# Performance work log

Hardware: AMD Instinct MI355X
Metric: run time of the kernel (lower is better)

The kernel has to match this reference:

```python
import jax, jax.numpy as jnp
import numpy as np

SIG_LEVEL = 2
UNIT = 128
SEQ = 64
BATCH = 256
SIG_DIM = UNIT + UNIT ** 2  # truncated signature dim for level 2
LN_EPS = 1e-5


def _signature(path, level):
    """Truncated path signature up to `level` via Chen's relation.
    path: (B, T, d) -> (B, d + d^2 + ... + d^level).
    Each segment contributes exp(dx): level-m term dx^{outer m}/m!.
    """
    B, T, d = path.shape
    dx = path[:, 1:] - path[:, :-1]  # (B, T-1, d)
    init = [jnp.zeros((B, d ** k), dtype=path.dtype) for k in range(1, level + 1)]

    def step(S, dxt):  # S: list of (B, d^k); dxt: (B, d)
        # P[m] = dxt^{outer m} / m!, flattened (B, d^m)
        P = [jnp.ones((B, 1), dtype=dxt.dtype), dxt]
        for m in range(2, level + 1):
            P.append((P[-1][:, :, None] * dxt[:, None, :]).reshape(B, d ** m) / m)
        newS = []
        for k in range(1, level + 1):
            s = P[k]  # j = 0 term (S_0 = 1)
            for j in range(1, k + 1):
                s = s + (S[j - 1][:, :, None] * P[k - j][:, None, :]).reshape(B, d ** k)
            newS.append(s)
        return newS, None

    S, _ = jax.lax.scan(step, init, jnp.swapaxes(dx, 0, 1))
    return jnp.concatenate(S, axis=-1)


def _grn_softmax(sig, W2, b2, W1, b1, Wg, bg, Wv, bv, Ws, bs, gamma, beta):
    # TFT-style gated residual network with softmax output activation.
    h = jax.nn.elu(sig @ W2 + b2)          # (B, unit)
    h = h @ W1 + b1                        # (B, unit)
    glu = jax.nn.sigmoid(h @ Wg + bg) * (h @ Wv + bv)
    skip = sig @ Ws + bs                   # residual projection sig_dim -> unit
    y = skip + glu
    mu = jnp.mean(y, axis=-1, keepdims=True)
    var = jnp.var(y, axis=-1, keepdims=True)
    y = (y - mu) * jax.lax.rsqrt(var + LN_EPS) * gamma + beta
    return jax.nn.softmax(y, axis=-1)


def setup_inputs() -> dict:
    key = jax.random.key(0)
    ks = jax.random.split(key, 16)
    s = 0.02
    return {
        "inputs": jax.random.normal(ks[0], (BATCH, SEQ, UNIT), dtype=jnp.float32),
        "time_kernel": jnp.ones((SEQ, 1), dtype=jnp.float32),
        "Wd": jax.random.normal(ks[1], (UNIT, UNIT), dtype=jnp.float32) * s,
        "bd": jnp.zeros((UNIT,), dtype=jnp.float32),
        "W2": jax.random.normal(ks[2], (SIG_DIM, UNIT), dtype=jnp.float32) * s,
        "b2": jnp.zeros((UNIT,), dtype=jnp.float32),
        "W1": jax.random.normal(ks[3], (UNIT, UNIT), dtype=jnp.float32) * s,
        "b1": jnp.zeros((UNIT,), dtype=jnp.float32),
        "Wg": jax.random.normal(ks[4], (UNIT, UNIT), dtype=jnp.float32) * s,
        "bg": jnp.zeros((UNIT,), dtype=jnp.float32),
        "Wv": jax.random.normal(ks[5], (UNIT, UNIT), dtype=jnp.float32) * s,
        "bv": jnp.zeros((UNIT,), dtype=jnp.float32),
        "Ws": jax.random.normal(ks[6], (SIG_DIM, UNIT), dtype=jnp.float32) * s,
        "bs": jnp.zeros((UNIT,), dtype=jnp.float32),
        "gamma": jnp.ones((UNIT,), dtype=jnp.float32),
        "beta": jnp.zeros((UNIT,), dtype=jnp.float32),
    }


def reference(inputs, time_kernel, Wd, bd, W2, b2, W1, b1, Wg, bg, Wv, bv, Ws, bs, gamma, beta):
    x = time_kernel * inputs                         # (B, T, d) time weighting
    sig = _signature(x, SIG_LEVEL)                   # (B, sig_dim)
    weights = _grn_softmax(sig, W2, b2, W1, b1, Wg, bg, Wv, bv, Ws, bs, gamma, beta)  # (B, d)
    dense_out = x @ Wd + bd                          # (B, T, d); dropout is identity at eval
    return dense_out * weights[:, None, :]
```

## Files before the change

kernel.cpp:

```cpp
#include <hip/hip_runtime.h>
#include <math.h>

#define SD 16512
#define NCH 129
#define CHUNKP 32768
#define LN_EPS 1e-5f

typedef __attribute__((ext_vector_type(4))) float f32x4;
typedef __attribute__((ext_vector_type(8))) short bf16x8;

__device__ __forceinline__ unsigned bfpack(float lo, float hi) {
    unsigned a = __builtin_bit_cast(unsigned, lo);
    unsigned b = __builtin_bit_cast(unsigned, hi);
    a = (a + 0x7FFFu + ((a >> 16) & 1u)) >> 16;
    b = (b + 0x7FFFu + ((b >> 16) & 1u)) >> 16;
    return a | (b << 16);
}
__device__ __forceinline__ unsigned short bf1(float x) {
    unsigned a = __builtin_bit_cast(unsigned, x);
    return (unsigned short)((a + 0x7FFFu + ((a >> 16) & 1u)) >> 16);
}

__global__ __launch_bounds__(512) void k_sig(const float* __restrict__ x,
                                             const float* __restrict__ tk,
                                             const float* __restrict__ Wd,
                                             unsigned short* __restrict__ sig,
                                             unsigned short* __restrict__ xbf,
                                             unsigned short* __restrict__ WdTg) {
    __shared__ unsigned short Ut[128][72];
    __shared__ unsigned short DXt[128][72];
    __shared__ float tks[64];
    int tid = threadIdx.x;
    int b = blockIdx.x;

    if (b == 256) {
        int d = tid & 127, kh = tid >> 7;
        unsigned* dst = (unsigned*)WdTg;
        for (int kk = 0; kk < 32; kk += 2) {
            int k = kh * 32 + kk;
            float v0 = Wd[(size_t)k * 128 + d];
            float v1 = Wd[(size_t)(k + 1) * 128 + d];
            dst[d * 64 + (k >> 1)] = bfpack(v0, v1);
        }
        return;
    }

    if (tid < 64) tks[tid] = tk[tid];
    __syncthreads();

    const float* xb = x + (size_t)b * 8192;
    unsigned short* xbb = xbf + (size_t)b * 8192;
    int i = tid & 127, th = tid >> 7;

    float x0 = tks[0] * xb[i];
    float xa = tks[th * 16] * xb[(size_t)(th * 16) * 128 + i];
    #pragma unroll
    for (int tp = 0; tp < 8; ++tp) {
        int p = th * 8 + tp;
        int t0 = 2 * p;
        float xv = tks[t0 + 1] * xb[(size_t)(t0 + 1) * 128 + i];
        float dx0 = xv - xa, u0 = 0.5f * (xa + xv) - x0;
        float dx1, u1, xc;
        if (p == 31) { dx1 = 0.f; u1 = 0.f; xc = 0.f; }
        else {
            xc = tks[t0 + 2] * xb[(size_t)(t0 + 2) * 128 + i];
            dx1 = xc - xv; u1 = 0.5f * (xv + xc) - x0;
        }
        *(unsigned*)&Ut[i][t0]  = bfpack(u0, u1);
        *(unsigned*)&DXt[i][t0] = bfpack(dx0, dx1);
        xbb[(size_t)t0 * 128 + i]       = bf1(xa);
        xbb[(size_t)(t0 + 1) * 128 + i] = bf1(xv);
        if (p == 31) sig[(size_t)b * SD + i] = bf1(xv - x0);
        xa = xc;
    }
    __syncthreads();

    int w = tid >> 6, lane = tid & 63;
    int wm = w >> 2, wn = w & 3;
    int l15 = lane & 15, lg = lane >> 4;
    f32x4 acc[4][2];
    #pragma unroll
    for (int m = 0; m < 4; ++m)
        #pragma unroll
        for (int n = 0; n < 2; ++n) acc[m][n] = (f32x4){0.f, 0.f, 0.f, 0.f};

    #pragma unroll
    for (int ks = 0; ks < 2; ++ks) {
        bf16x8 af[4], bfv[2];
        #pragma unroll
        for (int m = 0; m < 4; ++m)
            af[m] = *(const bf16x8*)&Ut[wm * 64 + m * 16 + l15][ks * 32 + lg * 8];
        #pragma unroll
        for (int n = 0; n < 2; ++n)
            bfv[n] = *(const bf16x8*)&DXt[wn * 32 + n * 16 + l15][ks * 32 + lg * 8];
        #pragma unroll
        for (int m = 0; m < 4; ++m)
            #pragma unroll
            for (int n = 0; n < 2; ++n)
                acc[m][n] = __builtin_amdgcn_mfma_f32_16x16x32_bf16(af[m], bfv[n], acc[m][n], 0, 0, 0);
    }

    unsigned short* sp = sig + (size_t)b * SD + 128;
    #pragma unroll
    for (int m = 0; m < 4; ++m)
        #pragma unroll
        for (int n = 0; n < 2; ++n)
            #pragma unroll
            for (int rr = 0; rr < 4; ++rr)
                sp[(size_t)(wm * 64 + m * 16 + lg * 4 + rr) * 128 + wn * 32 + n * 16 + l15]
                    = bf1(acc[m][n][rr]);
}

__global__ __launch_bounds__(512, 2) void k_gemm(const unsigned short* __restrict__ sig,
                                                 const float* __restrict__ W2,
                                                 const float* __restrict__ Ws,
                                                 unsigned* __restrict__ partial_p) {
    __shared__ unsigned short As[256 * 128];
    __shared__ unsigned short Bs[64 * 128];

    int p = blockIdx.x;
    int xc = p & 7, o = p >> 3;
    int lid = (xc < 4 ? xc * 65 : 260 + (xc - 4) * 64) + o;
    int ch = lid >> 2, nt = lid & 3;
    const float* W = (nt < 2) ? W2 : Ws;
    int ntc = (nt & 1) * 64;
    int kb = ch * 128;

    int tid = threadIdx.x;

    {
        int row = tid >> 1, half = tid & 1;
        const unsigned short* src = sig + (size_t)row * SD + kb + half * 64;
        int sw = (row & 7) << 3;
        #pragma unroll
        for (int j = 0; j < 8; ++j) {
            uint4 v = *(const uint4*)(src + j * 8);
            int cu = (half * 64 + j * 8) ^ sw;
            *(uint4*)&As[row * 128 + cu] = v;
        }
    }
    {
        int k = tid >> 2, cq = (tid & 3) * 16;
        const float* wp = W + (size_t)(kb + k) * 128 + ntc + cq;
        float v[16];
        #pragma unroll
        for (int u = 0; u < 4; ++u) {
            f32x4 t = *(const f32x4*)(wp + u * 4);
            v[u * 4] = t[0]; v[u * 4 + 1] = t[1]; v[u * 4 + 2] = t[2]; v[u * 4 + 3] = t[3];
        }
        #pragma unroll
        for (int u = 0; u < 16; ++u) {
            int c = cq + u;
            Bs[c * 128 + (k ^ ((c & 7) << 3))] = bf1(v[u]);
        }
    }
    __syncthreads();

    int w = tid >> 6, lane = tid & 63;
    int l15 = lane & 15, lg = lane >> 4;
    int rbase = w * 32;

    f32x4 acc[2][4];
    #pragma unroll
    for (int m = 0; m < 2; ++m)
        #pragma unroll
        for (int n = 0; n < 4; ++n) acc[m][n] = (f32x4){0.f, 0.f, 0.f, 0.f};

    #pragma unroll
    for (int ks = 0; ks < 4; ++ks) {
        bf16x8 af[2], bfv[4];
        #pragma unroll
        for (int m = 0; m < 2; ++m) {
            int row = rbase + m * 16 + l15;
            af[m] = *(const bf16x8*)&As[row * 128 + ((ks * 32 + lg * 8) ^ ((row & 7) << 3))];
        }
        #pragma unroll
        for (int n = 0; n < 4; ++n) {
            int col = n * 16 + l15;
            bfv[n] = *(const bf16x8*)&Bs[col * 128 + ((ks * 32 + lg * 8) ^ ((col & 7) << 3))];
        }
        #pragma unroll
        for (int m = 0; m < 2; ++m)
            #pragma unroll
            for (int n = 0; n < 4; ++n)
                acc[m][n] = __builtin_amdgcn_mfma_f32_16x16x32_bf16(af[m], bfv[n], acc[m][n], 0, 0, 0);
    }

    unsigned* Pp = partial_p + (size_t)ch * CHUNKP + nt * 64;
    #pragma unroll
    for (int m = 0; m < 2; ++m)
        #pragma unroll
        for (int n = 0; n < 4; ++n) {
            int r0 = rbase + m * 16 + lg * 4;
            int cc = n * 16 + l15;
            Pp[(size_t)(r0 >> 1) * 256 + cc]       = bfpack(acc[m][n][0], acc[m][n][1]);
            Pp[(size_t)((r0 >> 1) + 1) * 256 + cc] = bfpack(acc[m][n][2], acc[m][n][3]);
        }
}

__global__ __launch_bounds__(512) void k_tail(const unsigned* __restrict__ partial_p,
                                              const unsigned short* __restrict__ xbf,
                                              const unsigned short* __restrict__ WdTg,
                                              const float* __restrict__ b2,
                                              const float* __restrict__ W1,
                                              const float* __restrict__ b1,
                                              const float* __restrict__ Wg,
                                              const float* __restrict__ bg,
                                              const float* __restrict__ Wv,
                                              const float* __restrict__ bv,
                                              const float* __restrict__ bs,
                                              const float* __restrict__ gamma,
                                              const float* __restrict__ beta,
                                              const float* __restrict__ bd,
                                              float* __restrict__ out) {
    __shared__ float hs[128], ss[128], h2s[128];
    __shared__ float red4[4][128], rtmp[2][256];
    __shared__ float ys[128], es[128], wts[128];

    int b = blockIdx.x, tid = threadIdx.x;
    int lane = tid & 63;
    int l15 = lane & 15, lg = lane >> 4;

    {
        int c = tid & 255, h = tid >> 8;
        float s = 0.f;
        const unsigned* Pp = partial_p + (size_t)(b >> 1) * 256 + c;
        bool hi = (b & 1) != 0;
        #pragma unroll 8
        for (int ch = h; ch < NCH; ch += 2) {
            unsigned u = Pp[(size_t)ch * CHUNKP];
            unsigned hw = hi ? (u & 0xffff0000u) : (u << 16);
            s += __builtin_bit_cast(float, hw);
        }
        rtmp[h][c] = s;
    }
    __syncthreads();
    if (tid < 256) {
        float rsum = rtmp[0][tid] + rtmp[1][tid];
        if (tid < 128) {
            float hp = rsum + b2[tid];
            hs[tid] = hp > 0.f ? hp : expm1f(hp);
        } else {
            ss[tid - 128] = rsum + bs[tid - 128];
        }
    }
    __syncthreads();

    int c = tid & 127;
    {
        int qt = tid >> 7;
        float s = 0.f;
        int kbq = qt * 32;
        #pragma unroll 8
        for (int k = 0; k < 32; ++k) s += hs[kbq + k] * W1[(size_t)(kbq + k) * 128 + c];
        red4[qt][c] = s;
    }
    __syncthreads();
    if (tid < 128)
        h2s[tid] = red4[0][tid] + red4[1][tid] + red4[2][tid] + red4[3][tid] + b1[tid];
    __syncthreads();
    {
        int idx = tid >> 7, sel = idx & 1, kh = idx >> 1;
        const float* Wx = sel ? Wv : Wg;
        float s = 0.f;
        int kbq = kh * 64;
        #pragma unroll 8
        for (int k = 0; k < 64; ++k) s += h2s[kbq + k] * Wx[(size_t)(kbq + k) * 128 + c];
        red4[idx][c] = s;
    }
    __syncthreads();
    if (tid < 128) {
        float g = 1.f / (1.f + expf(-(red4[0][c] + red4[2][c] + bg[c])));
        float v = red4[1][c] + red4[3][c] + bv[c];
        ys[c] = ss[c] + g * v;
    }
    __syncthreads();
    if (tid < 128) {
        float sum = 0.f, sq = 0.f;
        for (int k = 0; k < 128; ++k) { float v = ys[k]; sum += v; sq += v * v; }
        float mu = sum * (1.f / 128.f);
        float var = sq * (1.f / 128.f) - mu * mu;
        float rs = rsqrtf(var + LN_EPS);
        es[c] = (ys[c] - mu) * rs * gamma[c] + beta[c];
    }
    __syncthreads();
    if (tid < 128) {
        float m = -1e30f;
        for (int k = 0; k < 128; ++k) m = fmaxf(m, es[k]);
        ys[c] = expf(es[c] - m);
    }
    __syncthreads();
    if (tid < 128) {
        float se = 0.f;
        for (int k = 0; k < 128; ++k) se += ys[k];
        wts[c] = ys[c] / se;
    }
    __syncthreads();

    int w4 = tid >> 6;
    const unsigned short* xrow = xbf + (size_t)b * 8192;
    f32x4 dacc[4];
    #pragma unroll
    for (int fm = 0; fm < 4; ++fm) dacc[fm] = (f32x4){0.f, 0.f, 0.f, 0.f};
    #pragma unroll
    for (int ks = 0; ks < 4; ++ks) {
        bf16x8 av[4], bv2;
        #pragma unroll
        for (int fm = 0; fm < 4; ++fm)
            av[fm] = *(const bf16x8*)(xrow + (size_t)(fm * 16 + l15) * 128 + ks * 32 + lg * 8);
        bv2 = *(const bf16x8*)(WdTg + (size_t)(w4 * 16 + l15) * 128 + ks * 32 + lg * 8);
        #pragma unroll
        for (int fm = 0; fm < 4; ++fm)
            dacc[fm] = __builtin_amdgcn_mfma_f32_16x16x32_bf16(av[fm], bv2, dacc[fm], 0, 0, 0);
    }
    int dcol = w4 * 16 + l15;
    float bdv = bd[dcol], wtv = wts[dcol];
    #pragma unroll
    for (int fm = 0; fm < 4; ++fm)
        #pragma unroll
        for (int rr = 0; rr < 4; ++rr) {
            int t = fm * 16 + lg * 4 + rr;
            out[(size_t)b * 8192 + (size_t)t * 128 + dcol] = (dacc[fm][rr] + bdv) * wtv;
        }
}

extern "C" void kernel_launch(void* const* d_in, const int* in_sizes, int n_in,
                              void* d_out, int out_size, void* d_ws, size_t ws_size,
                              hipStream_t stream) {
    const float* inputs = (const float*)d_in[0];
    const float* tk     = (const float*)d_in[1];
    const float* Wd     = (const float*)d_in[2];
    const float* bd     = (const float*)d_in[3];
    const float* W2     = (const float*)d_in[4];
    const float* b2     = (const float*)d_in[5];
    const float* W1     = (const float*)d_in[6];
    const float* b1     = (const float*)d_in[7];
    const float* Wg     = (const float*)d_in[8];
    const float* bg     = (const float*)d_in[9];
    const float* Wv     = (const float*)d_in[10];
    const float* bv     = (const float*)d_in[11];
    const float* Wsk    = (const float*)d_in[12];
    const float* bs     = (const float*)d_in[13];
    const float* gamma  = (const float*)d_in[14];
    const float* beta   = (const float*)d_in[15];
    float* out = (float*)d_out;

    char* ws = (char*)d_ws;
    unsigned short* sig  = (unsigned short*)ws;
    unsigned* partial_p  = (unsigned*)(ws + 8454144);
    unsigned short* xbf  = (unsigned short*)(ws + 25362432);
    unsigned short* WdTg = (unsigned short*)(ws + 29556736);

    k_sig <<<257, 512, 0, stream>>>(inputs, tk, Wd, sig, xbf, WdTg);
    k_gemm<<<516, 512, 0, stream>>>(sig, W2, Wsk, partial_p);
    k_tail<<<256, 512, 0, stream>>>(partial_p, xbf, WdTg, b2, W1, b1, Wg, bg, Wv, bv,
                                    bs, gamma, beta, bd, out);
}
```

Baseline: 44.58 us.

## Retile split-K GEMM into 32 K-chunks with smaller M/N tiles

The signature-to-hidden GEMM now uses 32 K-chunks of 512 (the last chunk covers 640) instead of 129 chunks of 128. Each block computes a 128x32 output tile and loops over four or five 128-wide K sub-steps, so far fewer bf16 partials are written and then reduced in the tail kernel. The partial buffer is re-laid out so the tail reads 256-wide contiguous rows per chunk, and the workspace offsets shrink to match. In exchange each block does a serial K loop with two barriers per step and gets less MFMA work per wave, and the sig matrix is loaded by eight N-tile blocks instead of four.

```diff
diff --git a/kernel.cpp b/kernel.cpp
--- a/kernel.cpp
+++ b/kernel.cpp
@@ -2,8 +2,8 @@
 #include <math.h>
 
 #define SD 16512
-#define NCH 129
-#define CHUNKP 32768
+#define NCH 32
+#define RPSTRIDE 8192
 #define LN_EPS 1e-5f
 
 typedef __attribute__((ext_vector_type(4))) float f32x4;
@@ -115,87 +115,86 @@
                                                  const float* __restrict__ W2,
                                                  const float* __restrict__ Ws,
                                                  unsigned* __restrict__ partial_p) {
-    __shared__ unsigned short As[256 * 128];
-    __shared__ unsigned short Bs[64 * 128];
+    __shared__ unsigned short As[128 * 128];
+    __shared__ unsigned short Bs[32 * 128];
 
     int p = blockIdx.x;
-    int xc = p & 7, o = p >> 3;
-    int lid = (xc < 4 ? xc * 65 : 260 + (xc - 4) * 64) + o;
-    int ch = lid >> 2, nt = lid & 3;
-    const float* W = (nt < 2) ? W2 : Ws;
-    int ntc = (nt & 1) * 64;
-    int kb = ch * 128;
+    int lid = (p & 7) * 64 + (p >> 3);
+    int ch = lid >> 4;
+    int mt = (lid >> 3) & 1;
+    int nt = lid & 7;
+    const float* W = (nt < 4) ? W2 : Ws;
+    int ntc = (nt & 3) * 32;
+    int kb0 = ch * 512;
+    int nsub = (ch == 31) ? 5 : 4;
 
     int tid = threadIdx.x;
-
-    {
-        int row = tid >> 1, half = tid & 1;
-        const unsigned short* src = sig + (size_t)row * SD + kb + half * 64;
-        int sw = (row & 7) << 3;
-        #pragma unroll
-        for (int j = 0; j < 8; ++j) {
-            uint4 v = *(const uint4*)(src + j * 8);
-            int cu = (half * 64 + j * 8) ^ sw;
-            *(uint4*)&As[row * 128 + cu] = v;
-        }
-    }
-    {
-        int k = tid >> 2, cq = (tid & 3) * 16;
-        const float* wp = W + (size_t)(kb + k) * 128 + ntc + cq;
-        float v[16];
-        #pragma unroll
-        for (int u = 0; u < 4; ++u) {
-            f32x4 t = *(const f32x4*)(wp + u * 4);
-            v[u * 4] = t[0]; v[u * 4 + 1] = t[1]; v[u * 4 + 2] = t[2]; v[u * 4 + 3] = t[3];
-        }
-        #pragma unroll
-        for (int u = 0; u < 16; ++u) {
-            int c = cq + u;
-            Bs[c * 128 + (k ^ ((c & 7) << 3))] = bf1(v[u]);
-        }
-    }
-    __syncthreads();
-
     int w = tid >> 6, lane = tid & 63;
     int l15 = lane & 15, lg = lane >> 4;
-    int rbase = w * 32;
-
-    f32x4 acc[2][4];
-    #pragma unroll
-    for (int m = 0; m < 2; ++m)
-        #pragma unroll
-        for (int n = 0; n < 4; ++n) acc[m][n] = (f32x4){0.f, 0.f, 0.f, 0.f};
-
-    #pragma unroll
-    for (int ks = 0; ks < 4; ++ks) {
-        bf16x8 af[2], bfv[4];
-        #pragma unroll
-        for (int m = 0; m < 2; ++m) {
-            int row = rbase + m * 16 + l15;
-            af[m] = *(const bf16x8*)&As[row * 128 + ((ks * 32 + lg * 8) ^ ((row & 7) << 3))];
-        }
-        #pragma unroll
-        for (int n = 0; n < 4; ++n) {
-            int col = n * 16 + l15;
-            bfv[n] = *(const bf16x8*)&Bs[col * 128 + ((ks * 32 + lg * 8) ^ ((col & 7) << 3))];
-        }
-        #pragma unroll
-        for (int m = 0; m < 2; ++m)
-            #pragma unroll
-            for (int n = 0; n < 4; ++n)
-                acc[m][n] = __builtin_amdgcn_mfma_f32_16x16x32_bf16(af[m], bfv[n], acc[m][n], 0, 0, 0);
-    }
-
-    unsigned* Pp = partial_p + (size_t)ch * CHUNKP + nt * 64;
-    #pragma unroll
-    for (int m = 0; m < 2; ++m)
-        #pragma unroll
-        for (int n = 0; n < 4; ++n) {
-            int r0 = rbase + m * 16 + lg * 4;
-            int cc = n * 16 + l15;
-            Pp[(size_t)(r0 >> 1) * 256 + cc]       = bfpack(acc[m][n][0], acc[m][n][1]);
-            Pp[(size_t)((r0 >> 1) + 1) * 256 + cc] = bfpack(acc[m][n][2], acc[m][n][3]);
-        }
+    const unsigned short* sigB = sig + (size_t)(mt * 128) * SD;
+
+    int arow = tid >> 2;
+    int aq   = (tid & 3) * 32;
+    int bk   = tid >> 2;
+    int bc0  = (tid & 3) * 8;
+
+    f32x4 acc[2];
+    acc[0] = (f32x4){0.f, 0.f, 0.f, 0.f};
+    acc[1] = (f32x4){0.f, 0.f, 0.f, 0.f};
+
+    for (int s = 0; s < nsub; ++s) {
+        int kb = kb0 + s * 128;
+        {
+            const unsigned short* src = sigB + (size_t)arow * SD + kb + aq;
+            int sw = (arow & 7) << 3;
+            #pragma unroll
+            for (int j = 0; j < 4; ++j) {
+                uint4 v = *(const uint4*)(src + j * 8);
+                *(uint4*)&As[arow * 128 + ((aq + j * 8) ^ sw)] = v;
+            }
+        }
+        {
+            const float* wp = W + (size_t)(kb + bk) * 128 + ntc + bc0;
+            f32x4 t0 = *(const f32x4*)wp;
+            f32x4 t1 = *(const f32x4*)(wp + 4);
+            float v[8] = {t0[0], t0[1], t0[2], t0[3], t1[0], t1[1], t1[2], t1[3]};
+            #pragma unroll
+            for (int u = 0; u < 8; ++u) {
+                int c = bc0 + u;
+                Bs[c * 128 + (bk ^ ((c & 7) << 3))] = bf1(v[u]);
+            }
+        }
+        __syncthreads();
+
+        #pragma unroll
+        for (int ks = 0; ks < 4; ++ks) {
+            int ko = ks * 32 + lg * 8;
+            bf16x8 af, bfv[2];
+            {
+                int row = w * 16 + l15;
+                af = *(const bf16x8*)&As[row * 128 + (ko ^ ((row & 7) << 3))];
+            }
+            #pragma unroll
+            for (int n = 0; n < 2; ++n) {
+                int col = n * 16 + l15;
+                bfv[n] = *(const bf16x8*)&Bs[col * 128 + (ko ^ ((col & 7) << 3))];
+            }
+            acc[0] = __builtin_amdgcn_mfma_f32_16x16x32_bf16(af, bfv[0], acc[0], 0, 0, 0);
+            acc[1] = __builtin_amdgcn_mfma_f32_16x16x32_bf16(af, bfv[1], acc[1], 0, 0, 0);
+        }
+        __syncthreads();
+    }
+
+    int r0 = mt * 128 + w * 16 + lg * 4;
+    int rp0 = r0 >> 1;
+    #pragma unroll
+    for (int n = 0; n < 2; ++n) {
+        int colg = nt * 32 + n * 16 + l15;
+        partial_p[(size_t)rp0 * RPSTRIDE + ch * 256 + colg]
+            = bfpack(acc[n][0], acc[n][1]);
+        partial_p[(size_t)(rp0 + 1) * RPSTRIDE + ch * 256 + colg]
+            = bfpack(acc[n][2], acc[n][3]);
+    }
 }
 
 __global__ __launch_bounds__(512) void k_tail(const unsigned* __restrict__ partial_p,
@@ -224,11 +223,11 @@
     {
         int c = tid & 255, h = tid >> 8;
         float s = 0.f;
-        const unsigned* Pp = partial_p + (size_t)(b >> 1) * 256 + c;
+        const unsigned* Pp = partial_p + (size_t)(b >> 1) * RPSTRIDE + c;
         bool hi = (b & 1) != 0;
         #pragma unroll 8
         for (int ch = h; ch < NCH; ch += 2) {
-            unsigned u = Pp[(size_t)ch * CHUNKP];
+            unsigned u = Pp[ch * 256];
             unsigned hw = hi ? (u & 0xffff0000u) : (u << 16);
             s += __builtin_bit_cast(float, hw);
         }
@@ -348,11 +347,11 @@
     char* ws = (char*)d_ws;
     unsigned short* sig  = (unsigned short*)ws;
     unsigned* partial_p  = (unsigned*)(ws + 8454144);
-    unsigned short* xbf  = (unsigned short*)(ws + 25362432);
-    unsigned short* WdTg = (unsigned short*)(ws + 29556736);
+    unsigned short* xbf  = (unsigned short*)(ws + 12648448);
+    unsigned short* WdTg = (unsigned short*)(ws + 16842752);
 
     k_sig <<<257, 512, 0, stream>>>(inputs, tk, Wd, sig, xbf, WdTg);
-    k_gemm<<<516, 512, 0, stream>>>(sig, W2, Wsk, partial_p);
+    k_gemm<<<512, 512, 0, stream>>>(sig, W2, Wsk, partial_p);
     k_tail<<<256, 512, 0, stream>>>(partial_p, xbf, WdTg, b2, W1, b1, Wg, bg, Wv, bv,
                                     bs, gamma, beta, bd, out);
 }
```

After: 40.24 us. 9.7% less time.
